# Kernel optimization log

Measured on AMD Instinct MI355X. Metric: run time of the kernel, lower is better.

Reference implementation:

```python
import jax, jax.numpy as jnp
import numpy as np

B = 262144
G = 3           # n_goods
HDIM = 256
IN = G * 2 + 1  # 7


def setup_inputs() -> dict:
    key = jax.random.key(0)
    ks = jax.random.split(key, 10)
    inp = {
        "log_p": jax.random.normal(ks[0], (B, G), jnp.float32),
        "log_y": jax.random.normal(ks[1], (B, 1), jnp.float32),
        "log_xb_prev": jax.random.normal(ks[2], (B, G), jnp.float32),
        "log_q_prev": jax.random.normal(ks[3], (B, G), jnp.float32),
        # Linear weights stored torch-style: (out, in)
        "W1": jax.random.normal(ks[4], (HDIM, IN), jnp.float32) * np.sqrt(2.0 / IN),
        "b1": jnp.zeros((HDIM,), jnp.float32),
        "W2": jax.random.normal(ks[5], (HDIM, HDIM), jnp.float32) * np.sqrt(2.0 / HDIM),
        "b2": jnp.zeros((HDIM,), jnp.float32),
        "W3": jax.random.normal(ks[6], (HDIM // 2, HDIM), jnp.float32) * np.sqrt(2.0 / HDIM),
        "b3": jnp.zeros((HDIM // 2,), jnp.float32),
        "W4": jax.random.uniform(ks[7], (G, HDIM // 2), jnp.float32,
                                  minval=-0.1 * np.sqrt(6.0 / (G + HDIM // 2)),
                                  maxval=0.1 * np.sqrt(6.0 / (G + HDIM // 2))),
        "b4": jnp.zeros((G,), jnp.float32),
        "log_beta": jnp.float32(1.5),
        "log_delta": jnp.float32(np.log(0.7 / 0.3)),
    }
    return inp


def reference(log_p, log_y, log_xb_prev, log_q_prev,
              W1, b1, W2, b2, W3, b3, W4, b4, log_beta, log_delta):
    beta = jnp.clip(jnp.exp(log_beta), 0.5, 20.0)
    delta = jax.nn.sigmoid(log_delta)
    xb = delta * log_xb_prev + (1.0 - delta) * log_q_prev      # (B, G)
    x = jnp.concatenate([log_p, log_y, xb], axis=1)            # (B, 2G+1)
    h = jax.nn.silu(x @ W1.T + b1)                             # (B, 256)
    h = jax.nn.silu(h @ W2.T + b2)                             # (B, 256)
    h = jax.nn.silu(h @ W3.T + b3)                             # (B, 128)
    logits = (h @ W4.T + b4) * beta                            # (B, G)
    return jax.nn.softmax(logits, axis=1)
```

## Files before the change

kernel.cpp:

```cpp
#include <hip/hip_runtime.h>
#include <hip/hip_bf16.h>

#define B_TOTAL 262144
#define G 3
#define HD 256
#define HD2 128
#define ROWS 128
#define NTHREADS 512
#define LDH 264

typedef short short8 __attribute__((ext_vector_type(8)));
typedef float floatx4 __attribute__((ext_vector_type(4)));

__device__ __forceinline__ unsigned short f2bf(float f) {
    unsigned u = __builtin_bit_cast(unsigned, f);
    u += 0x7FFFu + ((u >> 16) & 1u);
    return (unsigned short)(u >> 16);
}

__device__ __forceinline__ unsigned pack_bf16x2(float a, float b) {
#if __has_builtin(__builtin_amdgcn_cvt_pk_bf16_f32)
    auto r = __builtin_amdgcn_cvt_pk_bf16_f32(a, b);
    unsigned u;
    __builtin_memcpy(&u, &r, 4);
    return u;
#else
    return (unsigned)f2bf(a) | ((unsigned)f2bf(b) << 16);
#endif
}

__device__ __forceinline__ float fast_rcp(float x) {
#if __has_builtin(__builtin_amdgcn_rcpf)
    return __builtin_amdgcn_rcpf(x);
#else
    return 1.0f / x;
#endif
}
__device__ __forceinline__ float silu_f(float x) {
    return x * fast_rcp(1.0f + __expf(-x));
}

__global__ void convert_w_kernel(const float* __restrict__ W1, const float* __restrict__ W2,
                                 const float* __restrict__ W3, const float* __restrict__ W4,
                                 unsigned short* __restrict__ w1bf, unsigned short* __restrict__ w2bf,
                                 unsigned short* __restrict__ w3bf, unsigned short* __restrict__ w4bf) {
    int i = blockIdx.x * 256 + threadIdx.x;
    if (i < HD * HD)  w2bf[i] = f2bf(W2[i]);
    if (i < HD2 * HD) w3bf[i] = f2bf(W3[i]);
    if (i < HD * 32) { int r = i >> 5, k = i & 31; w1bf[i] = (k < 7) ? f2bf(W1[r * 7 + k]) : (unsigned short)0; }
    if (i < 16 * HD2) { int r = i >> 7, k = i & 127; w4bf[i] = (r < G) ? f2bf(W4[r * HD2 + k]) : (unsigned short)0; }
}

__global__ __launch_bounds__(NTHREADS, 4) void mlp_kernel(
    const float* __restrict__ log_p, const float* __restrict__ log_y,
    const float* __restrict__ log_xb, const float* __restrict__ log_q,
    const float* __restrict__ b1, const float* __restrict__ b2,
    const float* __restrict__ b3, const float* __restrict__ b4,
    const float* __restrict__ p_log_beta, const float* __restrict__ p_log_delta,
    const unsigned short* __restrict__ w1bf, const unsigned short* __restrict__ w2bf,
    const unsigned short* __restrict__ w3bf, const unsigned short* __restrict__ w4bf,
    float* __restrict__ out)
{
    __shared__ __align__(16) unsigned short hA[ROWS][LDH];
    __shared__ __align__(16) unsigned short x_bf[ROWS][8];
    __shared__ __align__(16) float bias1_s[HD];
    __shared__ __align__(16) float bias2_s[HD];
    __shared__ __align__(16) float bias3_s[HD2];

    const int tid  = threadIdx.x;
    const int lane = tid & 63;
    const int wv   = tid >> 6;
    const int quad = lane >> 4;
    const int l15  = lane & 15;
    const int row0 = blockIdx.x * ROWS;

    const float beta  = fminf(fmaxf(__expf(p_log_beta[0]), 0.5f), 20.0f);
    const float delta = fast_rcp(1.0f + __expf(-p_log_delta[0]));

    if (tid < HD) { bias1_s[tid] = b1[tid]; bias2_s[tid] = b2[tid]; }
    if (tid < HD2) bias3_s[tid] = b3[tid];
    if (tid < ROWS) {
        const int r = row0 + tid;
        const float p0 = log_p[r * 3 + 0], p1 = log_p[r * 3 + 1], p2 = log_p[r * 3 + 2];
        const float y  = log_y[r];
        const float xb0 = delta * log_xb[r * 3 + 0] + (1.0f - delta) * log_q[r * 3 + 0];
        const float xb1 = delta * log_xb[r * 3 + 1] + (1.0f - delta) * log_q[r * 3 + 1];
        const float xb2 = delta * log_xb[r * 3 + 2] + (1.0f - delta) * log_q[r * 3 + 2];
        uint4 u0;
        u0.x = pack_bf16x2(p0, p1);
        u0.y = pack_bf16x2(p2, y);
        u0.z = pack_bf16x2(xb0, xb1);
        u0.w = pack_bf16x2(xb2, 0.0f);
        *(uint4*)&x_bf[tid][0] = u0;
    }
    __syncthreads();

    #define EPILOGUE(ACC, M, N0)                                                   \
        {                                                                          \
            const float v0 = silu_f((ACC)[0]);                                     \
            const float v1 = silu_f((ACC)[1]);                                     \
            const float v2 = silu_f((ACC)[2]);                                     \
            const float v3 = silu_f((ACC)[3]);                                     \
            uint2 u; u.x = pack_bf16x2(v0, v1); u.y = pack_bf16x2(v2, v3);         \
            *(uint2*)&hA[(M)][(N0)] = u;                                           \
        }

    {
        const int nbase = wv * 32;
        short8 aw[2];
        #pragma unroll
        for (int nt = 0; nt < 2; ++nt)
            aw[nt] = *(const short8*)(w1bf + (nbase + nt * 16 + l15) * 32 + quad * 8);
        #pragma unroll
        for (int half = 0; half < 2; ++half) {
            short8 bx[4];
            #pragma unroll
            for (int mt = 0; mt < 4; ++mt) {
                if (quad == 0)
                    bx[mt] = *(const short8*)&x_bf[(half * 4 + mt) * 16 + l15][0];
                else
                    bx[mt] = (short8){0, 0, 0, 0, 0, 0, 0, 0};
            }
            #pragma unroll
            for (int nt = 0; nt < 2; ++nt) {
                const float4 bv = *(const float4*)&bias1_s[nbase + nt * 16 + quad * 4];
                #pragma unroll
                for (int mt = 0; mt < 4; ++mt) {
                    floatx4 acc = (floatx4){bv.x, bv.y, bv.z, bv.w};
                    acc = __builtin_amdgcn_mfma_f32_16x16x32_bf16(aw[nt], bx[mt], acc, 0, 0, 0);
                    EPILOGUE(acc, (half * 4 + mt) * 16 + l15, nbase + nt * 16 + quad * 4);
                }
            }
        }
    }
    __syncthreads();

    {
        const int nbase = wv * 32;
        floatx4 acc[8][2];
        #pragma unroll
        for (int nt = 0; nt < 2; ++nt) {
            const float4 bv = *(const float4*)&bias2_s[nbase + nt * 16 + quad * 4];
            #pragma unroll
            for (int mt = 0; mt < 8; ++mt)
                acc[mt][nt] = (floatx4){bv.x, bv.y, bv.z, bv.w};
        }
        short8 aw[2][2];
        #pragma unroll
        for (int nt = 0; nt < 2; ++nt)
            aw[0][nt] = *(const short8*)(w2bf + (nbase + nt * 16 + l15) * HD + quad * 8);
        #pragma unroll
        for (int ks = 0; ks < 8; ++ks) {
            const int cur = ks & 1, nxt = cur ^ 1;
            if (ks < 7) {
                const int kb = (ks + 1) * 32 + quad * 8;
                #pragma unroll
                for (int nt = 0; nt < 2; ++nt)
                    aw[nxt][nt] = *(const short8*)(w2bf + (nbase + nt * 16 + l15) * HD + kb);
            }
            const int kb0 = ks * 32 + quad * 8;
            #pragma unroll
            for (int chunk = 0; chunk < 2; ++chunk) {
                short8 bh[4];
                #pragma unroll
                for (int m = 0; m < 4; ++m)
                    bh[m] = *(const short8*)&hA[(chunk * 4 + m) * 16 + l15][kb0];
                #pragma unroll
                for (int m = 0; m < 4; ++m)
                    #pragma unroll
                    for (int nt = 0; nt < 2; ++nt)
                        acc[chunk * 4 + m][nt] = __builtin_amdgcn_mfma_f32_16x16x32_bf16(
                            aw[cur][nt], bh[m], acc[chunk * 4 + m][nt], 0, 0, 0);
            }
        }
        __syncthreads();
        #pragma unroll
        for (int mt = 0; mt < 8; ++mt) {
            #pragma unroll
            for (int nt = 0; nt < 2; ++nt)
                EPILOGUE(acc[mt][nt], mt * 16 + l15, nbase + nt * 16 + quad * 4);
        }
    }
    __syncthreads();

    {
        const int nbase = wv * 16;
        floatx4 acc[8];
        {
            const float4 bv = *(const float4*)&bias3_s[nbase + quad * 4];
            #pragma unroll
            for (int mt = 0; mt < 8; ++mt)
                acc[mt] = (floatx4){bv.x, bv.y, bv.z, bv.w};
        }
        short8 aw[2];
        aw[0] = *(const short8*)(w3bf + (nbase + l15) * HD + quad * 8);
        #pragma unroll
        for (int ks = 0; ks < 8; ++ks) {
            const int cur = ks & 1, nxt = cur ^ 1;
            if (ks < 7) {
                const int kb = (ks + 1) * 32 + quad * 8;
                aw[nxt] = *(const short8*)(w3bf + (nbase + l15) * HD + kb);
            }
            const int kb0 = ks * 32 + quad * 8;
            #pragma unroll
            for (int chunk = 0; chunk < 2; ++chunk) {
                short8 bh[4];
                #pragma unroll
                for (int m = 0; m < 4; ++m)
                    bh[m] = *(const short8*)&hA[(chunk * 4 + m) * 16 + l15][kb0];
                #pragma unroll
                for (int m = 0; m < 4; ++m)
                    acc[chunk * 4 + m] = __builtin_amdgcn_mfma_f32_16x16x32_bf16(
                        aw[cur], bh[m], acc[chunk * 4 + m], 0, 0, 0);
            }
        }
        __syncthreads();
        #pragma unroll
        for (int mt = 0; mt < 8; ++mt)
            EPILOGUE(acc[mt], mt * 16 + l15, nbase + quad * 4);
    }
    __syncthreads();

    {
        floatx4 acc;
        #pragma unroll
        for (int i = 0; i < 4; ++i) {
            const int rrow = quad * 4 + i;
            acc[i] = (rrow < G) ? b4[rrow] : 0.0f;
        }
        #pragma unroll
        for (int ks = 0; ks < 4; ++ks) {
            const int kb = ks * 32 + quad * 8;
            const short8 aw4 = *(const short8*)(w4bf + l15 * HD2 + kb);
            const short8 bh4 = *(const short8*)&hA[wv * 16 + l15][kb];
            acc = __builtin_amdgcn_mfma_f32_16x16x32_bf16(aw4, bh4, acc, 0, 0, 0);
        }
        if (lane < 16) {
            const float l0 = acc[0] * beta;
            const float l1 = acc[1] * beta;
            const float l2 = acc[2] * beta;
            const float m  = fmaxf(l0, fmaxf(l1, l2));
            const float e0 = __expf(l0 - m), e1 = __expf(l1 - m), e2 = __expf(l2 - m);
            const float inv = fast_rcp(e0 + e1 + e2);
            const int r = row0 + wv * 16 + l15;
            out[r * 3 + 0] = e0 * inv;
            out[r * 3 + 1] = e1 * inv;
            out[r * 3 + 2] = e2 * inv;
        }
    }
    #undef EPILOGUE
}

extern "C" void kernel_launch(void* const* d_in, const int* in_sizes, int n_in,
                              void* d_out, int out_size, void* d_ws, size_t ws_size,
                              hipStream_t stream) {
    (void)in_sizes; (void)n_in; (void)out_size; (void)ws_size;
    const float* log_p  = (const float*)d_in[0];
    const float* log_y  = (const float*)d_in[1];
    const float* log_xb = (const float*)d_in[2];
    const float* log_q  = (const float*)d_in[3];
    const float* W1 = (const float*)d_in[4];
    const float* b1 = (const float*)d_in[5];
    const float* W2 = (const float*)d_in[6];
    const float* b2 = (const float*)d_in[7];
    const float* W3 = (const float*)d_in[8];
    const float* b3 = (const float*)d_in[9];
    const float* W4 = (const float*)d_in[10];
    const float* b4 = (const float*)d_in[11];
    const float* lb = (const float*)d_in[12];
    const float* ld = (const float*)d_in[13];

    unsigned short* w2bf = (unsigned short*)d_ws;
    unsigned short* w3bf = w2bf + HD * HD;
    unsigned short* w1bf = w3bf + HD2 * HD;
    unsigned short* w4bf = w1bf + HD * 32;

    convert_w_kernel<<<256, 256, 0, stream>>>(W1, W2, W3, W4, w1bf, w2bf, w3bf, w4bf);
    mlp_kernel<<<B_TOTAL / ROWS, NTHREADS, 0, stream>>>(
        log_p, log_y, log_xb, log_q, b1, b2, b3, b4, lb, ld,
        w1bf, w2bf, w3bf, w4bf, (float*)d_out);
}
```

Baseline: 167.8 us.

## Double rows per block to 256 and remap waves to 16-column slabs

The block now processes 256 rows with 1024 threads (16 waves) instead of 128 rows with 512 threads. In layers 1 and 2 each wave owns a 16-wide output slab across all 256 rows, so one weight fragment is reused over 16 M-tiles instead of two fragments over 8. Layer 3 splits the waves into two 128-row halves. The aim is to amortise weight fetches and barriers over more rows. The cost is a larger LDS activation buffer, which likely limits residency to one block per CU, and more accumulator registers per wave in layer 2.

```diff
diff --git a/kernel.cpp b/kernel.cpp
--- a/kernel.cpp
+++ b/kernel.cpp
@@ -5,8 +5,8 @@
 #define G 3
 #define HD 256
 #define HD2 128
-#define ROWS 128
-#define NTHREADS 512
+#define ROWS 256
+#define NTHREADS 1024
 #define LDH 264
 
 typedef short short8 __attribute__((ext_vector_type(8)));
@@ -106,85 +106,70 @@
         }
 
     {
-        const int nbase = wv * 32;
-        short8 aw[2];
-        #pragma unroll
-        for (int nt = 0; nt < 2; ++nt)
-            aw[nt] = *(const short8*)(w1bf + (nbase + nt * 16 + l15) * 32 + quad * 8);
-        #pragma unroll
-        for (int half = 0; half < 2; ++half) {
+        const int nbase = wv * 16;
+        const short8 aw = *(const short8*)(w1bf + (nbase + l15) * 32 + quad * 8);
+        const float4 bv = *(const float4*)&bias1_s[nbase + quad * 4];
+        #pragma unroll
+        for (int chunk = 0; chunk < 4; ++chunk) {
             short8 bx[4];
             #pragma unroll
             for (int mt = 0; mt < 4; ++mt) {
                 if (quad == 0)
-                    bx[mt] = *(const short8*)&x_bf[(half * 4 + mt) * 16 + l15][0];
+                    bx[mt] = *(const short8*)&x_bf[(chunk * 4 + mt) * 16 + l15][0];
                 else
                     bx[mt] = (short8){0, 0, 0, 0, 0, 0, 0, 0};
             }
             #pragma unroll
-            for (int nt = 0; nt < 2; ++nt) {
-                const float4 bv = *(const float4*)&bias1_s[nbase + nt * 16 + quad * 4];
-                #pragma unroll
-                for (int mt = 0; mt < 4; ++mt) {
-                    floatx4 acc = (floatx4){bv.x, bv.y, bv.z, bv.w};
-                    acc = __builtin_amdgcn_mfma_f32_16x16x32_bf16(aw[nt], bx[mt], acc, 0, 0, 0);
-                    EPILOGUE(acc, (half * 4 + mt) * 16 + l15, nbase + nt * 16 + quad * 4);
-                }
-            }
-        }
-    }
-    __syncthreads();
-
-    {
-        const int nbase = wv * 32;
-        floatx4 acc[8][2];
-        #pragma unroll
-        for (int nt = 0; nt < 2; ++nt) {
-            const float4 bv = *(const float4*)&bias2_s[nbase + nt * 16 + quad * 4];
-            #pragma unroll
-            for (int mt = 0; mt < 8; ++mt)
-                acc[mt][nt] = (floatx4){bv.x, bv.y, bv.z, bv.w};
-        }
-        short8 aw[2][2];
-        #pragma unroll
-        for (int nt = 0; nt < 2; ++nt)
-            aw[0][nt] = *(const short8*)(w2bf + (nbase + nt * 16 + l15) * HD + quad * 8);
+            for (int mt = 0; mt < 4; ++mt) {
+                floatx4 acc = (floatx4){bv.x, bv.y, bv.z, bv.w};
+                acc = __builtin_amdgcn_mfma_f32_16x16x32_bf16(aw, bx[mt], acc, 0, 0, 0);
+                EPILOGUE(acc, (chunk * 4 + mt) * 16 + l15, nbase + quad * 4);
+            }
+        }
+    }
+    __syncthreads();
+
+    {
+        const int nbase = wv * 16;
+        floatx4 acc[16];
+        {
+            const float4 bv = *(const float4*)&bias2_s[nbase + quad * 4];
+            #pragma unroll
+            for (int mt = 0; mt < 16; ++mt)
+                acc[mt] = (floatx4){bv.x, bv.y, bv.z, bv.w};
+        }
+        short8 aw[2];
+        aw[0] = *(const short8*)(w2bf + (nbase + l15) * HD + quad * 8);
         #pragma unroll
         for (int ks = 0; ks < 8; ++ks) {
             const int cur = ks & 1, nxt = cur ^ 1;
             if (ks < 7) {
                 const int kb = (ks + 1) * 32 + quad * 8;
-                #pragma unroll
-                for (int nt = 0; nt < 2; ++nt)
-                    aw[nxt][nt] = *(const short8*)(w2bf + (nbase + nt * 16 + l15) * HD + kb);
+                aw[nxt] = *(const short8*)(w2bf + (nbase + l15) * HD + kb);
             }
             const int kb0 = ks * 32 + quad * 8;
             #pragma unroll
-            for (int chunk = 0; chunk < 2; ++chunk) {
+            for (int chunk = 0; chunk < 4; ++chunk) {
                 short8 bh[4];
                 #pragma unroll
                 for (int m = 0; m < 4; ++m)
                     bh[m] = *(const short8*)&hA[(chunk * 4 + m) * 16 + l15][kb0];
                 #pragma unroll
                 for (int m = 0; m < 4; ++m)
-                    #pragma unroll
-                    for (int nt = 0; nt < 2; ++nt)
-                        acc[chunk * 4 + m][nt] = __builtin_amdgcn_mfma_f32_16x16x32_bf16(
-                            aw[cur][nt], bh[m], acc[chunk * 4 + m][nt], 0, 0, 0);
+                    acc[chunk * 4 + m] = __builtin_amdgcn_mfma_f32_16x16x32_bf16(
+                        aw[cur], bh[m], acc[chunk * 4 + m], 0, 0, 0);
             }
         }
         __syncthreads();
         #pragma unroll
-        for (int mt = 0; mt < 8; ++mt) {
-            #pragma unroll
-            for (int nt = 0; nt < 2; ++nt)
-                EPILOGUE(acc[mt][nt], mt * 16 + l15, nbase + nt * 16 + quad * 4);
-        }
-    }
-    __syncthreads();
-
-    {
-        const int nbase = wv * 16;
+        for (int mt = 0; mt < 16; ++mt)
+            EPILOGUE(acc[mt], mt * 16 + l15, nbase + quad * 4);
+    }
+    __syncthreads();
+
+    {
+        const int nbase = (wv & 7) * 16;
+        const int mbase = (wv >> 3) * 128;
         floatx4 acc[8];
         {
             const float4 bv = *(const float4*)&bias3_s[nbase + quad * 4];
@@ -207,7 +192,7 @@
                 short8 bh[4];
                 #pragma unroll
                 for (int m = 0; m < 4; ++m)
-                    bh[m] = *(const short8*)&hA[(chunk * 4 + m) * 16 + l15][kb0];
+                    bh[m] = *(const short8*)&hA[mbase + (chunk * 4 + m) * 16 + l15][kb0];
                 #pragma unroll
                 for (int m = 0; m < 4; ++m)
                     acc[chunk * 4 + m] = __builtin_amdgcn_mfma_f32_16x16x32_bf16(
@@ -217,7 +202,7 @@
         __syncthreads();
         #pragma unroll
         for (int mt = 0; mt < 8; ++mt)
-            EPILOGUE(acc[mt], mt * 16 + l15, nbase + quad * 4);
+            EPILOGUE(acc[mt], mbase + mt * 16 + l15, nbase + quad * 4);
     }
     __syncthreads();
 
```

Result: slower. 192.8 us (+14.9%).
